# Kernel tuning notes

Hardware: AMD Instinct MI355X
Metric: run time of the kernel (lower is better)

## Reference

```python
import jax, jax.numpy as jnp
import numpy as np
import math

N, S, T, D = 4, 2048, 2048, 1024

def setup_inputs() -> dict:
    key = jax.random.key(0)
    ks = jax.random.split(key, 6)
    scale = 1.0 / math.sqrt(D)
    return {
        "query": jax.random.normal(ks[0], (N, S, D), dtype=jnp.float32),
        "key": jax.random.normal(ks[1], (N, T, D), dtype=jnp.float32),
        "value": jax.random.normal(ks[2], (N, T, D), dtype=jnp.float32),
        # causal mask: 1 = attend, 0 = masked out (masked_fill where mask == 0)
        "attn_mask": jnp.tril(jnp.ones((S, T), dtype=jnp.int32)),
        "Wq": jax.random.normal(ks[3], (D, D), dtype=jnp.float32) * scale,
        "Wk": jax.random.normal(ks[4], (D, D), dtype=jnp.float32) * scale,
        "Wv": jax.random.normal(ks[5], (D, D), dtype=jnp.float32) * scale,
    }

def reference(query, key, value, attn_mask, Wq, Wk, Wv):
    # nn.Linear(bias=False): y = x @ W.T
    q = jnp.einsum('nsd,ed->nse', query, Wq)
    k = jnp.einsum('ntd,ed->nte', key, Wk)
    v = jnp.einsum('ntd,ed->nte', value, Wv)
    # scaled dot-product scores [N, S, T]
    dot = jnp.einsum('nse,nte->nst', q, k) / jnp.sqrt(jnp.asarray(D, q.dtype))
    dot = jnp.where(attn_mask == 0, -jnp.inf, dot)
    scores = jax.nn.softmax(dot, axis=-1)
    # dropout is identity in eval mode
    y = jnp.einsum('nst,nte->nse', scores, v)
    return y
```

## Files before the change

kernel.cpp:

```cpp
#include <hip/hip_runtime.h>
#include <math.h>

using u16 = unsigned short;
typedef __attribute__((ext_vector_type(8))) __bf16 bf16x8;
typedef __attribute__((ext_vector_type(4))) float f32x4;
typedef __attribute__((ext_vector_type(4))) float f4v;
typedef __attribute__((ext_vector_type(8))) u16 u16x8;

__device__ __forceinline__ u16 f2bf(float f) {
  unsigned u = __float_as_uint(f);
  u += 0x7fffu + ((u >> 16) & 1u);
  return (u16)(u >> 16);
}
__device__ __forceinline__ float bf2f(u16 b) {
  unsigned u = ((unsigned)b) << 16;
  return __uint_as_float(u);
}

__device__ __forceinline__ void gload16(const void* g, void* l) {
  __builtin_amdgcn_global_load_lds(
      (const __attribute__((address_space(1))) unsigned int*)g,
      (__attribute__((address_space(3))) unsigned int*)l, 16, 0, 0);
}

__device__ __forceinline__ f32x4 MF(bf16x8 a, bf16x8 b, f32x4 c) {
  return __builtin_amdgcn_mfma_f32_16x16x32_bf16(a, b, c, 0, 0, 0);
}

#define BARX() __builtin_amdgcn_s_barrier()
#define LGKM0() asm volatile("s_waitcnt lgkmcnt(0)" ::: "memory")
#define VMW4() asm volatile("s_waitcnt vmcnt(4)" ::: "memory")
#define VMW0() asm volatile("s_waitcnt vmcnt(0)" ::: "memory")

__global__ __launch_bounds__(256) void prep(
    const float* __restrict__ q, const float* __restrict__ v,
    const float* __restrict__ k, const float* __restrict__ Wk,
    const float* __restrict__ Wq, const float* __restrict__ Wv,
    u16* __restrict__ qb, u16* __restrict__ wkT, u16* __restrict__ wqT,
    u16* __restrict__ wv_bf) {
  __shared__ float t[64][65];
  int b = blockIdx.x;
  if (b < 12288) {
    int z = b >> 12;
    int bb = b & 4095;
    const float* in = (z == 0) ? q : (z == 1) ? v : k;
    size_t i = ((size_t)bb * 256 + threadIdx.x) * 8;
    f4v a = *reinterpret_cast<const f4v*>(in + i);
    f4v c = *reinterpret_cast<const f4v*>(in + i + 4);
    u16x8 r;
    r[0] = f2bf(a[0]); r[1] = f2bf(a[1]); r[2] = f2bf(a[2]); r[3] = f2bf(a[3]);
    r[4] = f2bf(c[0]); r[5] = f2bf(c[1]); r[6] = f2bf(c[2]); r[7] = f2bf(c[3]);
    *reinterpret_cast<u16x8*>(qb + (size_t)z * 8388608 + i) = r;
  } else if (b < 12800) {
    int c = b - 12288;
    int z = c >> 8, idx = c & 255;
    const float* I = z ? Wq : Wk;
    u16* O = z ? wqT : wkT;
    int c0 = (idx & 15) * 64, r0 = (idx >> 4) * 64;
    int tx = threadIdx.x & 63, ty = threadIdx.x >> 6;
    #pragma unroll
    for (int i = 0; i < 64; i += 4)
      t[ty + i][tx] = I[(size_t)(r0 + ty + i) * 1024 + c0 + tx];
    __syncthreads();
    #pragma unroll
    for (int i = 0; i < 64; i += 4)
      O[(size_t)(c0 + ty + i) * 1024 + r0 + tx] = f2bf(t[tx][ty + i]);
  } else {
    int bb = b - 12800;
    size_t i = (size_t)bb * 4096 + threadIdx.x * 16;
    #pragma unroll
    for (int h = 0; h < 2; ++h) {
      f4v a = *reinterpret_cast<const f4v*>(Wv + i + h * 8);
      f4v c = *reinterpret_cast<const f4v*>(Wv + i + h * 8 + 4);
      u16x8 r;
      r[0] = f2bf(a[0]); r[1] = f2bf(a[1]); r[2] = f2bf(a[2]); r[3] = f2bf(a[3]);
      r[4] = f2bf(c[0]); r[5] = f2bf(c[1]); r[6] = f2bf(c[2]); r[7] = f2bf(c[3]);
      *reinterpret_cast<u16x8*>(wv_bf + i + h * 8) = r;
    }
  }
}

__global__ __launch_bounds__(512, 1) void proj256(
    const u16* __restrict__ Xq, const u16* __restrict__ Xv,
    const u16* __restrict__ Mt, const u16* __restrict__ Wv,
    u16* __restrict__ Yq, u16* __restrict__ Vt) {
  int h = blockIdx.x;
  int l = (h & 7) * 32 + (h >> 3);
  const bool wV = l >= 128;
  int li = l & 127;
  int bm, bn;
  const u16 *Ag, *Bg;
  if (!wV) {
    bm = li >> 2; bn = li & 3;
    Ag = Xq + (size_t)bm * 256 * 1024;
    Bg = Mt + (size_t)bn * 256 * 1024;
  } else {
    bm = li & 3; bn = li >> 2;
    Ag = Wv + (size_t)bm * 256 * 1024;
    Bg = Xv + (size_t)bn * 256 * 1024;
  }

  __shared__ __align__(16) char sm[131072];

  const int tid = threadIdx.x;
  const int lane = tid & 63, wv = tid >> 6;
  const int wr = wv >> 2, wc = wv & 3;
  const int fr = lane & 15, hi = lane >> 4, fr7 = lane & 7;
  const int l3 = lane >> 3;
  const int colsw = ((lane & 7) ^ l3) * 8;
  const int lnx16 = lane * 16;

  const u16 *pA[2][2], *pB[2][2];
  int ldsA[2][2], ldsB[2][2];
  #pragma unroll
  for (int hh = 0; hh < 2; ++hh)
    #pragma unroll
    for (int j = 0; j < 2; ++j) {
      int row = hh * 128 + wv * 8 + j * 64 + l3;
      pA[hh][j] = Ag + (size_t)row * 1024 + colsw;
      pB[hh][j] = Bg + (size_t)row * 1024 + colsw;
      ldsA[hh][j] = hh * 16384 + (wv + j * 8) * 1024 + lnx16;
      ldsB[hh][j] = 32768 + ldsA[hh][j];
    }

  const int aBase = wr * 16384 + fr * 128;
  const int bBase = 32768 + (wc >> 1) * 16384 + ((wc & 1) * 64 + fr) * 128;
  const int sl0 = (hi ^ fr7) << 4;
  const int sl1 = ((4 + hi) ^ fr7) << 4;

#define RDA(buf, m, kk) (*(const bf16x8*)((buf) + aBase + (m) * 2048 + ((kk) ? sl1 : sl0)))
#define RDB(buf, n, kk) (*(const bf16x8*)((buf) + bBase + (n) * 2048 + ((kk) ? sl1 : sl0)))

  f32x4 acc[8][4] = {};
  const int nt = 16;

  {
    char* b0 = sm;
    gload16(pA[0][0], b0 + ldsA[0][0]); gload16(pA[0][1], b0 + ldsA[0][1]);
    gload16(pA[1][0], b0 + ldsA[1][0]); gload16(pA[1][1], b0 + ldsA[1][1]);
    gload16(pB[0][0], b0 + ldsB[0][0]); gload16(pB[0][1], b0 + ldsB[0][1]);
    gload16(pB[1][0], b0 + ldsB[1][0]); gload16(pB[1][1], b0 + ldsB[1][1]);
    char* b1 = sm + 65536;
    gload16(pB[0][0] + 64, b1 + ldsB[0][0]); gload16(pB[0][1] + 64, b1 + ldsB[0][1]);
    gload16(pB[1][0] + 64, b1 + ldsB[1][0]); gload16(pB[1][1] + 64, b1 + ldsB[1][1]);
  }
  VMW4();
  BARX();

  for (int t = 0; t < nt; ++t) {
    const int cur = t & 1;
    const char* buf = sm + cur * 65536;
    char* nbuf = sm + (cur ^ 1) * 65536;
    char* cbuf = sm + cur * 65536;
    const bool st1 = (t + 1 < nt), st2 = (t + 2 < nt);
    bf16x8 bf0[4], bf1[4];
    bf16x8 a00, a01, a10, a11;

    a00 = RDA(buf, 0, 0); a01 = RDA(buf, 0, 1);
    a10 = RDA(buf, 1, 0); a11 = RDA(buf, 1, 1);
    #pragma unroll
    for (int n = 0; n < 4; ++n) { bf0[n] = RDB(buf, n, 0); bf1[n] = RDB(buf, n, 1); }
    if (st1) {
      gload16(pA[0][0] + (t + 1) * 64, nbuf + ldsA[0][0]);
      gload16(pA[0][1] + (t + 1) * 64, nbuf + ldsA[0][1]);
    }
    BARX(); LGKM0();
    __builtin_amdgcn_s_setprio(1);
    #pragma unroll
    for (int n = 0; n < 4; ++n) {
      acc[0][n] = MF(a00, bf0[n], acc[0][n]);
      acc[0][n] = MF(a01, bf1[n], acc[0][n]);
      acc[1][n] = MF(a10, bf0[n], acc[1][n]);
      acc[1][n] = MF(a11, bf1[n], acc[1][n]);
    }
    __builtin_amdgcn_s_setprio(0);
    BARX();

    a00 = RDA(buf, 2, 0); a01 = RDA(buf, 2, 1);
    a10 = RDA(buf, 3, 0); a11 = RDA(buf, 3, 1);
    if (st1) {
      gload16(pA[1][0] + (t + 1) * 64, nbuf + ldsA[1][0]);
      gload16(pA[1][1] + (t + 1) * 64, nbuf + ldsA[1][1]);
    }
    if (st2) {
      gload16(pB[0][0] + (t + 2) * 64, cbuf + ldsB[0][0]);
      gload16(pB[0][1] + (t + 2) * 64, cbuf + ldsB[0][1]);
    }
    BARX(); LGKM0();
    __builtin_amdgcn_s_setprio(1);
    #pragma unroll
    for (int n = 0; n < 4; ++n) {
      acc[2][n] = MF(a00, bf0[n], acc[2][n]);
      acc[2][n] = MF(a01, bf1[n], acc[2][n]);
      acc[3][n] = MF(a10, bf0[n], acc[3][n]);
      acc[3][n] = MF(a11, bf1[n], acc[3][n]);
    }
    __builtin_amdgcn_s_setprio(0);
    BARX();

    a00 = RDA(buf, 4, 0); a01 = RDA(buf, 4, 1);
    a10 = RDA(buf, 5, 0); a11 = RDA(buf, 5, 1);
    if (st2) {
      gload16(pB[1][0] + (t + 2) * 64, cbuf + ldsB[1][0]);
      gload16(pB[1][1] + (t + 2) * 64, cbuf + ldsB[1][1]);
    }
    BARX(); LGKM0();
    __builtin_amdgcn_s_setprio(1);
    #pragma unroll
    for (int n = 0; n < 4; ++n) {
      acc[4][n] = MF(a00, bf0[n], acc[4][n]);
      acc[4][n] = MF(a01, bf1[n], acc[4][n]);
      acc[5][n] = MF(a10, bf0[n], acc[5][n]);
      acc[5][n] = MF(a11, bf1[n], acc[5][n]);
    }
    __builtin_amdgcn_s_setprio(0);
    BARX();

    a00 = RDA(buf, 6, 0); a01 = RDA(buf, 6, 1);
    a10 = RDA(buf, 7, 0); a11 = RDA(buf, 7, 1);
    if (st2) { VMW4(); } else if (st1) { VMW0(); }
    BARX(); LGKM0();
    __builtin_amdgcn_s_setprio(1);
    #pragma unroll
    for (int n = 0; n < 4; ++n) {
      acc[6][n] = MF(a00, bf0[n], acc[6][n]);
      acc[6][n] = MF(a01, bf1[n], acc[6][n]);
      acc[7][n] = MF(a10, bf0[n], acc[7][n]);
      acc[7][n] = MF(a11, bf1[n], acc[7][n]);
    }
    __builtin_amdgcn_s_setprio(0);
    BARX();
  }

  if (!wV) {
    const int row0 = bm * 256 + wr * 128 + hi * 4;
    const int col0 = bn * 256 + wc * 64 + fr;
    #pragma unroll
    for (int m = 0; m < 8; ++m)
      #pragma unroll
      for (int n = 0; n < 4; ++n)
        #pragma unroll
        for (int j = 0; j < 4; ++j)
          Yq[(size_t)(row0 + m * 16 + j) * 1024 + (col0 + n * 16)] =
              f2bf(acc[m][n][j]);
  } else {
    const int e0 = bm * 256 + wr * 128 + hi * 4;
    const int t0 = (bn & 7) * 256 + wc * 64 + fr;
    const size_t zoff = (size_t)(bn >> 3) * (1024 * 2048);
    #pragma unroll
    for (int m = 0; m < 8; ++m)
      #pragma unroll
      for (int n = 0; n < 4; ++n)
        #pragma unroll
        for (int j = 0; j < 4; ++j)
          Vt[zoff + (size_t)(e0 + m * 16 + j) * 2048 + (t0 + n * 16)] =
              f2bf(acc[m][n][j]);
  }
#undef RDA
#undef RDB
}

template<typename OutT, int MODE>
__global__ __launch_bounds__(512) void gemm_bt8(
    const u16* __restrict__ A, const u16* __restrict__ B, OutT* __restrict__ C,
    int K, int lda, int ldb, int ldc,
    size_t sA, size_t sB, size_t sC, float alpha) {
  int bn, bm, bz = 0;
  int kEnd = K;
  if (MODE == 0) {
    bm = blockIdx.x >> 3;
    bn = blockIdx.x & 7;
  } else if (MODE == 1) {
    int h = blockIdx.x;
    int l = (h & 7) * 68 + (h >> 3);
    bz = l / 136;
    int t = l % 136;
    bm = (int)((sqrtf(8.f * (float)t + 1.f) - 1.f) * 0.5f);
    while ((bm + 1) * (bm + 2) / 2 <= t) ++bm;
    while (bm * (bm + 1) / 2 > t) --bm;
    bn = t - bm * (bm + 1) / 2;
  } else {
    int l = blockIdx.x;
    bm = 15 - (l >> 5);
    int rest = l & 31;
    bz = rest >> 3;
    bn = rest & 7;
    kEnd = (K < (bm + 1) * 128) ? K : (bm + 1) * 128;
  }
  const u16* Ag = A + sA * bz + (size_t)bm * 128 * lda;
  const u16* Bg = B + sB * bz + (size_t)bn * 128 * ldb;
  OutT* Cg = C + sC * bz;

  __shared__ __align__(16) u16 As[2][128 * 32];
  __shared__ __align__(16) u16 Bs[2][128 * 32];

  const int tid = threadIdx.x;
  const int lane = tid & 63, wv = tid >> 6;
  const int wr = wv >> 2, wc = wv & 3;
  const int fr = lane & 15, kq = (lane >> 4) * 8;
  const int g4 = (lane >> 4) * 4;

  const int e0 = wv * 512 + lane * 8;
  const int r0 = e0 >> 5, c0 = e0 & 31;
  const u16* a0 = Ag + (size_t)r0 * lda + c0;
  const u16* b0 = Bg + (size_t)r0 * ldb + c0;

  f32x4 acc[4][2] = {};
  const int nt = kEnd / 32;

  gload16(a0, &As[0][wv * 512]);
  gload16(b0, &Bs[0][wv * 512]);
  __syncthreads();

  for (int t = 0; t < nt; ++t) {
    const int cur = t & 1;
    if (t + 1 < nt) {
      const int k0 = (t + 1) * 32;
      gload16(a0 + k0, &As[cur ^ 1][wv * 512]);
      gload16(b0 + k0, &Bs[cur ^ 1][wv * 512]);
    }
    bf16x8 af[4], bfv[2];
    #pragma unroll
    for (int m = 0; m < 4; ++m)
      af[m] = *reinterpret_cast<const bf16x8*>(&As[cur][(wr * 64 + m * 16 + fr) * 32 + kq]);
    #pragma unroll
    for (int n = 0; n < 2; ++n)
      bfv[n] = *reinterpret_cast<const bf16x8*>(&Bs[cur][(wc * 32 + n * 16 + fr) * 32 + kq]);
    #pragma unroll
    for (int m = 0; m < 4; ++m)
      #pragma unroll
      for (int n = 0; n < 2; ++n)
        acc[m][n] = MF(af[m], bfv[n], acc[m][n]);
    __syncthreads();
  }

  const int row0 = bm * 128 + wr * 64 + g4;
  const int col0 = bn * 128 + wc * 32 + fr;
  #pragma unroll
  for (int m = 0; m < 4; ++m)
    #pragma unroll
    for (int n = 0; n < 2; ++n) {
      #pragma unroll
      for (int j = 0; j < 4; ++j) {
        float val = acc[m][n][j] * alpha;
        size_t idx = (size_t)(row0 + m * 16 + j) * ldc + (col0 + n * 16);
        if constexpr (sizeof(OutT) == 2) Cg[idx] = f2bf(val);
        else Cg[idx] = val;
      }
    }
}

__global__ __launch_bounds__(256) void softmax_causal(u16* __restrict__ sc) {
  int r = blockIdx.x;
  int s = r & 2047;
  u16* row = sc + (size_t)r * 2048;
  int tid = threadIdx.x;
  int t0 = tid * 8;
  u16x8 raw = {0, 0, 0, 0, 0, 0, 0, 0};
  if (t0 <= s) raw = *reinterpret_cast<const u16x8*>(row + t0);
  float v[8];
  float mx = -1e30f;
  #pragma unroll
  for (int j = 0; j < 8; ++j) {
    v[j] = ((t0 + j) <= s) ? bf2f(raw[j]) : -1e30f;
    mx = fmaxf(mx, v[j]);
  }
  #pragma unroll
  for (int o = 32; o; o >>= 1) mx = fmaxf(mx, __shfl_xor(mx, o, 64));
  __shared__ float red[8];
  if ((tid & 63) == 0) red[tid >> 6] = mx;
  __syncthreads();
  mx = fmaxf(fmaxf(red[0], red[1]), fmaxf(red[2], red[3]));
  float p[8];
  float sum = 0.f;
  #pragma unroll
  for (int j = 0; j < 8; ++j) {
    p[j] = ((t0 + j) <= s) ? __expf(v[j] - mx) : 0.f;
    sum += p[j];
  }
  #pragma unroll
  for (int o = 32; o; o >>= 1) sum += __shfl_xor(sum, o, 64);
  if ((tid & 63) == 0) red[4 + (tid >> 6)] = sum;
  __syncthreads();
  sum = red[4] + red[5] + red[6] + red[7];
  float inv = 1.0f / sum;
  u16x8 o8;
  #pragma unroll
  for (int j = 0; j < 8; ++j) o8[j] = f2bf(p[j] * inv);
  if (t0 <= (s | 127))
    *reinterpret_cast<u16x8*>(row + t0) = o8;
}

extern "C" void kernel_launch(void* const* d_in, const int* in_sizes, int n_in,
                              void* d_out, int out_size, void* d_ws, size_t ws_size,
                              hipStream_t stream) {
  const float* q  = (const float*)d_in[0];
  const float* k  = (const float*)d_in[1];
  const float* v  = (const float*)d_in[2];
  const float* Wq = (const float*)d_in[4];
  const float* Wk = (const float*)d_in[5];
  const float* Wv = (const float*)d_in[6];
  float* out = (float*)d_out;
  char* ws = (char*)d_ws;

  const size_t MB = 1024ull * 1024ull;
  u16* sc   = (u16*)ws;
  u16* qb   = (u16*)ws;
  u16* xk   = (u16*)(ws + 32 * MB);
  u16* wsl  = (u16*)(ws + 48 * MB);
  u16* wkT  = (u16*)(ws + 52 * MB);
  u16* wqT  = (u16*)(ws + 54 * MB);
  u16* Vt   = (u16*)(ws + 56 * MB);
  u16* Yq   = (u16*)(ws + 72 * MB);
  (void)in_sizes; (void)n_in; (void)out_size; (void)ws_size;

  prep<<<13056, 256, 0, stream>>>(q, v, k, Wk, Wq, Wv, qb, wkT, wqT,
                                  wsl + 1048576);

  gemm_bt8<u16, 0><<<64, 512, 0, stream>>>(
      wkT, wqT, wsl, 1024, 1024, 1024, 1024, 0, 0, 0, 1.0f);

  proj256<<<256, 512, 0, stream>>>(qb, qb + 8388608, wsl, wsl + 1048576,
                                   Yq, Vt);

  gemm_bt8<u16, 1><<<544, 512, 0, stream>>>(
      Yq, xk, sc, 1024, 1024, 1024, 2048,
      (size_t)2048 * 1024, (size_t)2048 * 1024, (size_t)2048 * 2048, 0.03125f);

  softmax_causal<<<8192, 256, 0, stream>>>(sc);

  gemm_bt8<float, 2><<<512, 512, 0, stream>>>(
      sc, Vt, out, 2048, 2048, 2048, 1024,
      (size_t)2048 * 2048, (size_t)1024 * 2048, (size_t)2048 * 1024, 1.0f);
}
```

Baseline: 162.0 us.

## Fuse causal softmax into QK and PV GEMM epilogues with atomic row sums

Removes the standalone softmax kernel. The QK^T GEMM epilogue now writes exp(score) with causal masking and accumulates per-row sums into a workspace buffer via atomics. The PV GEMM epilogue divides by those row sums. The aim is to save a full read and write pass over the score matrix plus one launch. It drops max subtraction, so it relies on scores staying small enough not to overflow in exp. The prep kernel also converts 16 elements per thread instead of 8 and zeroes the row-sum buffer.

```diff
diff --git a/kernel.cpp b/kernel.cpp
--- a/kernel.cpp
+++ b/kernel.cpp
@@ -12,10 +12,6 @@
   u += 0x7fffu + ((u >> 16) & 1u);
   return (u16)(u >> 16);
 }
-__device__ __forceinline__ float bf2f(u16 b) {
-  unsigned u = ((unsigned)b) << 16;
-  return __uint_as_float(u);
-}
 
 __device__ __forceinline__ void gload16(const void* g, void* l) {
   __builtin_amdgcn_global_load_lds(
@@ -37,22 +33,28 @@
     const float* __restrict__ k, const float* __restrict__ Wk,
     const float* __restrict__ Wq, const float* __restrict__ Wv,
     u16* __restrict__ qb, u16* __restrict__ wkT, u16* __restrict__ wqT,
-    u16* __restrict__ wv_bf) {
+    u16* __restrict__ wv_bf, float* __restrict__ lbuf) {
   __shared__ float t[64][65];
   int b = blockIdx.x;
-  if (b < 12288) {
-    int z = b >> 12;
-    int bb = b & 4095;
+  if (b < 6144) {
+    int z = b >> 11;
+    int bb = b & 2047;
     const float* in = (z == 0) ? q : (z == 1) ? v : k;
-    size_t i = ((size_t)bb * 256 + threadIdx.x) * 8;
-    f4v a = *reinterpret_cast<const f4v*>(in + i);
-    f4v c = *reinterpret_cast<const f4v*>(in + i + 4);
-    u16x8 r;
-    r[0] = f2bf(a[0]); r[1] = f2bf(a[1]); r[2] = f2bf(a[2]); r[3] = f2bf(a[3]);
-    r[4] = f2bf(c[0]); r[5] = f2bf(c[1]); r[6] = f2bf(c[2]); r[7] = f2bf(c[3]);
-    *reinterpret_cast<u16x8*>(qb + (size_t)z * 8388608 + i) = r;
-  } else if (b < 12800) {
-    int c = b - 12288;
+    size_t i = ((size_t)bb * 256 + threadIdx.x) * 16;
+    f4v a0 = *reinterpret_cast<const f4v*>(in + i);
+    f4v a1 = *reinterpret_cast<const f4v*>(in + i + 4);
+    f4v a2 = *reinterpret_cast<const f4v*>(in + i + 8);
+    f4v a3 = *reinterpret_cast<const f4v*>(in + i + 12);
+    u16x8 r0, r1;
+    r0[0] = f2bf(a0[0]); r0[1] = f2bf(a0[1]); r0[2] = f2bf(a0[2]); r0[3] = f2bf(a0[3]);
+    r0[4] = f2bf(a1[0]); r0[5] = f2bf(a1[1]); r0[6] = f2bf(a1[2]); r0[7] = f2bf(a1[3]);
+    r1[0] = f2bf(a2[0]); r1[1] = f2bf(a2[1]); r1[2] = f2bf(a2[2]); r1[3] = f2bf(a2[3]);
+    r1[4] = f2bf(a3[0]); r1[5] = f2bf(a3[1]); r1[6] = f2bf(a3[2]); r1[7] = f2bf(a3[3]);
+    u16* o = qb + (size_t)z * 8388608 + i;
+    *reinterpret_cast<u16x8*>(o) = r0;
+    *reinterpret_cast<u16x8*>(o + 8) = r1;
+  } else if (b < 6656) {
+    int c = b - 6144;
     int z = c >> 8, idx = c & 255;
     const float* I = z ? Wq : Wk;
     u16* O = z ? wqT : wkT;
@@ -65,8 +67,8 @@
     #pragma unroll
     for (int i = 0; i < 64; i += 4)
       O[(size_t)(c0 + ty + i) * 1024 + r0 + tx] = f2bf(t[tx][ty + i]);
-  } else {
-    int bb = b - 12800;
+  } else if (b < 6912) {
+    int bb = b - 6656;
     size_t i = (size_t)bb * 4096 + threadIdx.x * 16;
     #pragma unroll
     for (int h = 0; h < 2; ++h) {
@@ -77,6 +79,11 @@
       r[4] = f2bf(c[0]); r[5] = f2bf(c[1]); r[6] = f2bf(c[2]); r[7] = f2bf(c[3]);
       *reinterpret_cast<u16x8*>(wv_bf + i + h * 8) = r;
     }
+  } else {
+    f4v z4 = {0.f, 0.f, 0.f, 0.f};
+    #pragma unroll
+    for (int j = 0; j < 8; ++j)
+      *reinterpret_cast<f4v*>(&lbuf[threadIdx.x * 32 + j * 4]) = z4;
   }
 }
 
@@ -264,7 +271,7 @@
 __global__ __launch_bounds__(512) void gemm_bt8(
     const u16* __restrict__ A, const u16* __restrict__ B, OutT* __restrict__ C,
     int K, int lda, int ldb, int ldc,
-    size_t sA, size_t sB, size_t sC, float alpha) {
+    size_t sA, size_t sB, size_t sC, float alpha, float* __restrict__ lbuf) {
   int bn, bm, bz = 0;
   int kEnd = K;
   if (MODE == 0) {
@@ -334,6 +341,55 @@
     __syncthreads();
   }
 
+  if constexpr (MODE == 1) {
+    float psum[4][4];
+    #pragma unroll
+    for (int m = 0; m < 4; ++m)
+      #pragma unroll
+      for (int j = 0; j < 4; ++j) {
+        int tr = wr * 64 + g4 + m * 16 + j;
+        float rs = 0.f;
+        #pragma unroll
+        for (int n = 0; n < 2; ++n) {
+          int tc = wc * 32 + fr + n * 16;
+          float p = 0.f;
+          if (!(bm == bn && tc > tr)) p = __expf(acc[m][n][j] * alpha);
+          Cg[(size_t)(bm * 128 + tr) * ldc + (bn * 128 + tc)] = f2bf(p);
+          rs += p;
+        }
+        psum[m][j] = rs;
+      }
+    #pragma unroll
+    for (int o = 1; o < 16; o <<= 1)
+      #pragma unroll
+      for (int m = 0; m < 4; ++m)
+        #pragma unroll
+        for (int j = 0; j < 4; ++j)
+          psum[m][j] += __shfl_xor(psum[m][j], o, 64);
+    float* lsum = (float*)As;
+    if (fr == 0)
+      #pragma unroll
+      for (int m = 0; m < 4; ++m)
+        #pragma unroll
+        for (int j = 0; j < 4; ++j)
+          lsum[wc * 128 + wr * 64 + g4 + m * 16 + j] = psum[m][j];
+    __syncthreads();
+    if (tid < 128) {
+      float s = lsum[tid] + lsum[128 + tid] + lsum[256 + tid] + lsum[384 + tid];
+      atomicAdd(&lbuf[(size_t)bz * 2048 + bm * 128 + tid], s);
+    }
+    return;
+  }
+
+  float il[4][4];
+  if constexpr (MODE == 2) {
+    #pragma unroll
+    for (int m = 0; m < 4; ++m)
+      #pragma unroll
+      for (int j = 0; j < 4; ++j)
+        il[m][j] = 1.0f / lbuf[(size_t)bz * 2048 + bm * 128 + wr * 64 + g4 + m * 16 + j];
+  }
+
   const int row0 = bm * 128 + wr * 64 + g4;
   const int col0 = bn * 128 + wc * 32 + fr;
   #pragma unroll
@@ -342,53 +398,14 @@
     for (int n = 0; n < 2; ++n) {
       #pragma unroll
       for (int j = 0; j < 4; ++j) {
-        float val = acc[m][n][j] * alpha;
+        float val;
+        if constexpr (MODE == 2) val = acc[m][n][j] * il[m][j];
+        else val = acc[m][n][j] * alpha;
         size_t idx = (size_t)(row0 + m * 16 + j) * ldc + (col0 + n * 16);
         if constexpr (sizeof(OutT) == 2) Cg[idx] = f2bf(val);
         else Cg[idx] = val;
       }
     }
-}
-
-__global__ __launch_bounds__(256) void softmax_causal(u16* __restrict__ sc) {
-  int r = blockIdx.x;
-  int s = r & 2047;
-  u16* row = sc + (size_t)r * 2048;
-  int tid = threadIdx.x;
-  int t0 = tid * 8;
-  u16x8 raw = {0, 0, 0, 0, 0, 0, 0, 0};
-  if (t0 <= s) raw = *reinterpret_cast<const u16x8*>(row + t0);
-  float v[8];
-  float mx = -1e30f;
-  #pragma unroll
-  for (int j = 0; j < 8; ++j) {
-    v[j] = ((t0 + j) <= s) ? bf2f(raw[j]) : -1e30f;
-    mx = fmaxf(mx, v[j]);
-  }
-  #pragma unroll
-  for (int o = 32; o; o >>= 1) mx = fmaxf(mx, __shfl_xor(mx, o, 64));
-  __shared__ float red[8];
-  if ((tid & 63) == 0) red[tid >> 6] = mx;
-  __syncthreads();
-  mx = fmaxf(fmaxf(red[0], red[1]), fmaxf(red[2], red[3]));
-  float p[8];
-  float sum = 0.f;
-  #pragma unroll
-  for (int j = 0; j < 8; ++j) {
-    p[j] = ((t0 + j) <= s) ? __expf(v[j] - mx) : 0.f;
-    sum += p[j];
-  }
-  #pragma unroll
-  for (int o = 32; o; o >>= 1) sum += __shfl_xor(sum, o, 64);
-  if ((tid & 63) == 0) red[4 + (tid >> 6)] = sum;
-  __syncthreads();
-  sum = red[4] + red[5] + red[6] + red[7];
-  float inv = 1.0f / sum;
-  u16x8 o8;
-  #pragma unroll
-  for (int j = 0; j < 8; ++j) o8[j] = f2bf(p[j] * inv);
-  if (t0 <= (s | 127))
-    *reinterpret_cast<u16x8*>(row + t0) = o8;
 }
 
 extern "C" void kernel_launch(void* const* d_in, const int* in_sizes, int n_in,
@@ -412,24 +429,25 @@
   u16* wqT  = (u16*)(ws + 54 * MB);
   u16* Vt   = (u16*)(ws + 56 * MB);
   u16* Yq   = (u16*)(ws + 72 * MB);
+  float* lb = (float*)(ws + 88 * MB);
   (void)in_sizes; (void)n_in; (void)out_size; (void)ws_size;
 
-  prep<<<13056, 256, 0, stream>>>(q, v, k, Wk, Wq, Wv, qb, wkT, wqT,
-                                  wsl + 1048576);
+  prep<<<6913, 256, 0, stream>>>(q, v, k, Wk, Wq, Wv, qb, wkT, wqT,
+                                 wsl + 1048576, lb);
 
   gemm_bt8<u16, 0><<<64, 512, 0, stream>>>(
-      wkT, wqT, wsl, 1024, 1024, 1024, 1024, 0, 0, 0, 1.0f);
+      wkT, wqT, wsl, 1024, 1024, 1024, 1024, 0, 0, 0, 1.0f, nullptr);
 
   proj256<<<256, 512, 0, stream>>>(qb, qb + 8388608, wsl, wsl + 1048576,
                                    Yq, Vt);
 
   gemm_bt8<u16, 1><<<544, 512, 0, stream>>>(
       Yq, xk, sc, 1024, 1024, 1024, 2048,
-      (size_t)2048 * 1024, (size_t)2048 * 1024, (size_t)2048 * 2048, 0.03125f);
-
-  softmax_causal<<<8192, 256, 0, stream>>>(sc);
+      (size_t)2048 * 1024, (size_t)2048 * 1024, (size_t)2048 * 2048, 0.03125f,
+      lb);
 
   gemm_bt8<float, 2><<<512, 512, 0, stream>>>(
       sc, Vt, out, 2048, 2048, 2048, 1024,
-      (size_t)2048 * 2048, (size_t)1024 * 2048, (size_t)2048 * 1024, 1.0f);
-}
+      (size_t)2048 * 2048, (size_t)1024 * 2048, (size_t)2048 * 1024, 1.0f,
+      lb);
+}
```

Result: faster. 156.6 us, median of 3 (-3.3%).
